# Performance work log

Measured on AMD Instinct MI355X. Metric: run time of the kernel, lower is better.

The kernel has to match this reference:

```python
import jax, jax.numpy as jnp
import numpy as np
from jax import lax

REPR_IN = (32, 16, 8)   # multiplicities of l=0,1,2 fields
SIZE = 5                # cubic kernel size (odd)
PAD = SIZE // 2


def setup_inputs() -> dict:
    key = jax.random.key(0)
    k1, k2 = jax.random.split(key)
    c_in = sum(mul * (2 * l + 1) for l, mul in enumerate(REPR_IN))   # 120
    n_non_scalar = sum(REPR_IN[1:])                                   # 24
    x = jax.random.normal(k1, (2, c_in, 48, 48, 48), dtype=jnp.float32)
    # SE3Convolution materialized as its effective dense conv kernel [O, I, D, H, W]
    fan_in = c_in * SIZE ** 3
    w_gate = jax.random.normal(k2, (n_non_scalar, c_in, SIZE, SIZE, SIZE), dtype=jnp.float32) / np.sqrt(fan_in)
    return {"x": x, "w_gate": w_gate}


def reference(x, w_gate):
    B, _, X, Y, Z = x.shape
    # Gate branch: 3D conv (same padding) -> sigmoid, one scalar gate per non-scalar field
    g = jax.nn.sigmoid(
        lax.conv_general_dilated(
            x, w_gate,
            window_strides=(1, 1, 1),
            padding=[(PAD, PAD)] * 3,
            dimension_numbers=("NCDHW", "OIDHW", "NCDHW"),
        )
    )  # [B, n_non_scalar, X, Y, Z]

    parts = []
    begin_x = 0
    begin_g = 0
    for l, mul in enumerate(REPR_IN):
        if mul == 0:
            continue
        dim = 2 * l + 1
        field_x = x[:, begin_x:begin_x + mul * dim]
        if l == 0:
            # scalar activation on the l=0 block
            parts.append(jax.nn.relu(field_x))
        else:
            # broadcast gate over the 2l+1 components of each field copy
            fx = field_x.reshape(B, mul, dim, X, Y, Z)
            fg = g[:, begin_g:begin_g + mul][:, :, None]      # [B, mul, 1, X, Y, Z]
            begin_g += mul
            parts.append((fx * fg).reshape(B, mul * dim, X, Y, Z))
        begin_x += mul * dim
    return jnp.concatenate(parts, axis=1)
```

## Files before the change

kernel.cpp:

```cpp
#include <hip/hip_runtime.h>

typedef __attribute__((ext_vector_type(8))) short short8;
typedef __attribute__((ext_vector_type(4))) float f32x4;

#define SDIM 48
#define SS   (48*48)
#define SSS  (48*48*48)
#define CIN  120
#define CIP  128
#define NCO  24
#define ZP   52
#define NTAP 125

#define WP_USHORTS (4*25*5*32*32)
#define WP_BYTES   ((size_t)WP_USHORTS*2)
#define XT_USHORTS ((size_t)2*48*48*ZP*CIP)
#define XT_BYTES   (XT_USHORTS*2)
#define WTOT_F32   (NCO*CIN*NTAP)

#define A_CHUNKS 1664
#define ABUF_USH 13312
#define GLP      25

__device__ __forceinline__ unsigned short f2bf(float f){
    unsigned u = __float_as_uint(f);
    u = (u + 0x7FFFu + ((u >> 16) & 1u)) >> 16;
    return (unsigned short)u;
}

__device__ __forceinline__ void gload_lds16(const unsigned short* g, unsigned short* l)
{
    __builtin_amdgcn_global_load_lds(
        (const __attribute__((address_space(1))) unsigned int*)g,
        (__attribute__((address_space(3))) unsigned int*)l,
        16, 0, 0);
}


__global__ __launch_bounds__(256)
void transpose_x(const float* __restrict__ x, unsigned short* __restrict__ xt)
{
    __shared__ unsigned short sm[CIN*50];
    int bid = blockIdx.x;
    const int iy = bid % 48; bid /= 48;
    const int ix = bid % 48;
    const int b  = bid / 48;
    const int tid = threadIdx.x;

    const float* __restrict__ src = x + (size_t)b*CIN*SSS + ((size_t)ix*48 + iy)*48;
    for (int idx = tid; idx < CIN*48; idx += 256) {
        int ci = idx / 48, z = idx - ci*48;
        sm[ci*50 + z] = f2bf(src[(size_t)ci*SSS + z]);
    }
    __syncthreads();
    unsigned short* __restrict__ dst = xt + (((size_t)(b*48 + ix)*48) + iy)*ZP*CIP;
    for (int odx = tid; odx < ZP*CIP; odx += 256) {
        int zp = odx >> 7, ci = odx & 127;
        int z = zp - 2;
        unsigned short v = 0;
        if (ci < CIN && (unsigned)z < 48u) v = sm[ci*50 + z];
        dst[odx] = v;
    }
}

__global__ __launch_bounds__(256)
void repack_w_bf16(const float* __restrict__ w, unsigned short* __restrict__ wp)
{
    int idx = blockIdx.x*256 + threadIdx.x;
    if (idx >= WP_USHORTS) return;
    int cik = idx & 31;
    int co  = (idx >> 5) & 31;
    int dz  = (idx >> 10) % 5;
    int t   = (idx / 5120) % 25;
    int cc  = idx / 128000;
    int ci  = cc*32 + cik;
    float v = 0.f;
    if (co < NCO && ci < CIN)
        v = w[(size_t)(co*CIN + ci)*NTAP + t*5 + dz];
    wp[idx] = f2bf(v);
}

#define MFMA16(a,b,c) __builtin_amdgcn_mfma_f32_16x16x32_bf16(a,b,c,0,0,0)

__global__ __launch_bounds__(128, 3)
void conv_mfma(const unsigned short* __restrict__ xt,
               const unsigned short* __restrict__ wp,
               const float* __restrict__ x,
               float* __restrict__ out)
{
    __shared__ __align__(16) unsigned short As[ABUF_USH];

    int bid = (blockIdx.x & 7) * 144 + (blockIdx.x >> 3);
    const int oyq = bid % 12; bid /= 12;
    const int ox = bid % 48;
    const int b  = bid / 48;

    const int tid = threadIdx.x;
    const int wave = tid >> 6, lane = tid & 63;
    const int l15 = lane & 15, l4 = lane >> 4;
    const int iy0 = oyq*4 - 2;

    const int dxlo = (ox < 2) ? (2 - ox) : 0;
    const int dxhi = (ox > 45) ? (49 - ox) : 4;
    const int ndx  = dxhi - dxlo + 1;

    int goff[13];
    bool ok[13];
#pragma unroll
    for (int k = 0; k < 13; ++k) {
        int L = k*128 + tid;
        int iyl = L / 208, r = L - iyl*208;
        int zp = r >> 2, sf = r & 3;
        int sg = sf ^ ((zp >> 1) & 3);
        int iy = iy0 + iyl;
        ok[k]   = (unsigned)iy < 48u;
        goff[k] = (iy*52 + zp)*128 + sg*8;
    }
    const unsigned short* zsrc = xt + (lane & 31)*8;

    f32x4 acc[2][3][2];
#pragma unroll
    for (int oh = 0; oh < 2; ++oh)
#pragma unroll
      for (int zb = 0; zb < 3; ++zb)
#pragma unroll
        for (int nt = 0; nt < 2; ++nt) acc[oh][zb][nt] = (f32x4){0,0,0,0};

#pragma unroll 1
    for (int cc = 0; cc < 4; ++cc) {
#pragma unroll 1
      for (int dxi = 0; dxi < ndx; ++dxi) {
        const int dx = dxlo + dxi;
        const int ix = ox + dx - 2;
        const unsigned short* __restrict__ slab =
            xt + (size_t)(b*48 + ix)*(48*52*128) + cc*32;

        __syncthreads();
#pragma unroll
        for (int k = 0; k < 13; ++k) {
            const unsigned short* src = ok[k] ? (slab + goff[k]) : zsrc;
            gload_lds16(src, As + k*1024 + wave*512);
        }
        asm volatile("s_waitcnt vmcnt(0)" ::: "memory");
        __builtin_amdgcn_sched_barrier(0);
        __syncthreads();

        const unsigned short* __restrict__ wdxb =
            wp + (size_t)cc*128000 + (size_t)dx*25600 + l15*32 + l4*8;
        const char* __restrict__ asb = (const char*)As;
#pragma unroll
        for (int dz = 0; dz < 5; ++dz) {
            short8 bb[5][2];
#pragma unroll
            for (int dy = 0; dy < 5; ++dy) {
                bb[dy][0] = *(const short8*)(wdxb + dy*5120 + dz*1024);
                bb[dy][1] = *(const short8*)(wdxb + dy*5120 + dz*1024 + 512);
            }
#pragma unroll
            for (int r = 0; r < 6; ++r) {
                const char* __restrict__ ab = asb + (wave*2 + r)*3328;
                short8 a[3];
#pragma unroll
                for (int zb = 0; zb < 3; ++zb) {
                    const int zp = l15 + dz + zb*16;
                    const int off = zp*64 + ((l4 ^ ((zp >> 1) & 3)) << 4);
                    a[zb] = *(const short8*)(ab + off);
                }
                if (r <= 4) {
#pragma unroll
                    for (int zb = 0; zb < 3; ++zb) {
                        acc[0][zb][0] = MFMA16(a[zb], bb[r][0], acc[0][zb][0]);
                        acc[0][zb][1] = MFMA16(a[zb], bb[r][1], acc[0][zb][1]);
                    }
                }
                if (r >= 1) {
#pragma unroll
                    for (int zb = 0; zb < 3; ++zb) {
                        acc[1][zb][0] = MFMA16(a[zb], bb[r-1][0], acc[1][zb][0]);
                        acc[1][zb][1] = MFMA16(a[zb], bb[r-1][1], acc[1][zb][1]);
                    }
                }
            }
        }
      }
    }

    __syncthreads();
    float* gl = (float*)As;

#pragma unroll
    for (int nt = 0; nt < 2; ++nt) {
        const int co = nt*16 + l15;
        if (co < NCO) {
#pragma unroll
            for (int oh = 0; oh < 2; ++oh)
#pragma unroll
              for (int zb = 0; zb < 3; ++zb)
#pragma unroll
                for (int r = 0; r < 4; ++r) {
                    const int z0 = zb*16 + l4*4 + r;
                    gl[((wave*2 + oh)*48 + z0)*GLP + co] =
                        1.f / (1.f + __expf(-acc[oh][zb][nt][r]));
                }
        }
    }
    __syncthreads();

    for (int i = tid; i < 384; i += 128) {
        const int pnt = i % 192;
        const int half = i / 192;
        const int z = pnt % 48, oyl = pnt / 48;
        const int oy2 = oyq*4 + oyl;
        const size_t sp = ((size_t)ox*48 + oy2)*48 + z;
        const float* __restrict__ xsp = x   + (size_t)b*CIN*SSS + sp;
        float*       __restrict__ osp = out + (size_t)b*CIN*SSS + sp;
        const float* __restrict__ gp = gl + pnt*GLP;
        for (int c = half*60; c < half*60 + 60; ++c) {
            float v = xsp[(size_t)c*SSS];
            float o;
            if (c < 32)       o = v > 0.f ? v : 0.f;
            else if (c < 80)  o = v * gp[(c - 32) / 3];
            else              o = v * gp[16 + (c - 80) / 5];
            osp[(size_t)c*SSS] = o;
        }
    }
}


__global__ __launch_bounds__(256)
void repack_w_f32(const float* __restrict__ w, float* __restrict__ wpf)
{
    int idx = blockIdx.x * 256 + threadIdx.x;
    if (idx >= WTOT_F32) return;
    int co = idx % NCO;
    int t  = idx / NCO;
    wpf[idx] = w[co * (CIN * NTAP) + t];
}

__global__ __launch_bounds__(128)
void gated_act_f32(const float* __restrict__ x,
                   const float* __restrict__ wpf,
                   float* __restrict__ out)
{
    const int gid = blockIdx.x * 128 + threadIdx.x;
    const int oz = gid % SDIM;
    int r = gid / SDIM;
    const int oy = r % SDIM; r /= SDIM;
    const int ox = r % SDIM;
    const int b  = r / SDIM;

    const float* __restrict__ xb = x + (size_t)b * CIN * SSS;
    float acc[NCO];
#pragma unroll
    for (int i = 0; i < NCO; ++i) acc[i] = 0.f;

    int izc[5]; bool okz[5];
#pragma unroll
    for (int dz = 0; dz < 5; ++dz) {
        int iz = oz + dz - 2;
        okz[dz] = (unsigned)iz < (unsigned)SDIM;
        izc[dz] = okz[dz] ? iz : 0;
    }
    for (int ci = 0; ci < CIN; ++ci) {
        const float* __restrict__ xc = xb + (size_t)ci * SSS;
        const float* __restrict__ wc = wpf + ci * (NTAP * NCO);
#pragma unroll 1
        for (int dx = 0; dx < 5; ++dx) {
            const int ix = ox + dx - 2;
            const bool okx = (unsigned)ix < (unsigned)SDIM;
            const int ixc = okx ? ix : 0;
#pragma unroll 1
            for (int dy = 0; dy < 5; ++dy) {
                const int iy = oy + dy - 2;
                const bool oky = (unsigned)iy < (unsigned)SDIM;
                const int iyc = oky ? iy : 0;
                const bool okxy = okx && oky;
                const float* __restrict__ xrow = xc + ixc * SS + iyc * SDIM;
                float xv[5];
#pragma unroll
                for (int dz = 0; dz < 5; ++dz) {
                    float v = xrow[izc[dz]];
                    xv[dz] = (okxy && okz[dz]) ? v : 0.f;
                }
                const float* __restrict__ wr = wc + (dx * 25 + dy * 5) * NCO;
#pragma unroll
                for (int dz = 0; dz < 5; ++dz) {
                    const float v = xv[dz];
#pragma unroll
                    for (int co = 0; co < NCO; ++co)
                        acc[co] = fmaf(v, wr[dz * NCO + co], acc[co]);
                }
            }
        }
    }
    float g[NCO];
#pragma unroll
    for (int co = 0; co < NCO; ++co)
        g[co] = 1.f / (1.f + __expf(-acc[co]));

    const size_t sbase = (size_t)b * CIN * SSS + ox * SS + oy * SDIM + oz;
    float* __restrict__ ob = out + sbase;
    const float* __restrict__ xs = x + sbase;
#pragma unroll
    for (int c = 0; c < 32; ++c) {
        float v = xs[(size_t)c * SSS];
        ob[(size_t)c * SSS] = v > 0.f ? v : 0.f;
    }
#pragma unroll
    for (int m = 0; m < 16; ++m) {
        const float gv = g[m];
#pragma unroll
        for (int k = 0; k < 3; ++k) {
            const int c = 32 + m * 3 + k;
            ob[(size_t)c * SSS] = xs[(size_t)c * SSS] * gv;
        }
    }
#pragma unroll
    for (int m = 0; m < 8; ++m) {
        const float gv = g[16 + m];
#pragma unroll
        for (int k = 0; k < 5; ++k) {
            const int c = 80 + m * 5 + k;
            ob[(size_t)c * SSS] = xs[(size_t)c * SSS] * gv;
        }
    }
}

extern "C" void kernel_launch(void* const* d_in, const int* in_sizes, int n_in,
                              void* d_out, int out_size, void* d_ws, size_t ws_size,
                              hipStream_t stream)
{
    const float* x = (const float*)d_in[0];
    const float* w = (const float*)d_in[1];
    float* out = (float*)d_out;

    if (ws_size >= WP_BYTES + XT_BYTES) {
        unsigned short* wp  = (unsigned short*)d_ws;
        unsigned short* xtb = (unsigned short*)((char*)d_ws + WP_BYTES);
        hipLaunchKernelGGL(repack_w_bf16, dim3((WP_USHORTS + 255) / 256), dim3(256),
                           0, stream, w, wp);
        hipLaunchKernelGGL(transpose_x, dim3(2*48*48), dim3(256), 0, stream, x, xtb);
        hipLaunchKernelGGL(conv_mfma, dim3(2*48*12), dim3(128), 0, stream,
                           xtb, wp, x, out);
    } else if (ws_size >= (size_t)WTOT_F32 * 4) {
        float* wpf = (float*)d_ws;
        hipLaunchKernelGGL(repack_w_f32, dim3((WTOT_F32 + 255) / 256), dim3(256),
                           0, stream, w, wpf);
        hipLaunchKernelGGL(gated_act_f32, dim3(2*SSS/128), dim3(128), 0, stream,
                           x, wpf, out);
    }
}
```

Baseline: 319.9 us.

## Use single-wave conv blocks and drop block barriers in the staging loop

Each conv block shrinks from two waves covering four output rows to one wave covering two rows, doubling the grid to 2304 blocks. With a single wave per block the __syncthreads around the LDS staging go away. The next slab is now issued right after the MFMA work, and s_setprio raises wave priority during the MFMA section. The cost is more redundant halo rows and weight loads per output row. There is still only one LDS buffer, so loads overlap compute only across different waves, not within a block.

After: 452.7 us. +41.5%, slower.

```diff
diff --git a/kernel.cpp b/kernel.cpp
--- a/kernel.cpp
+++ b/kernel.cpp
@@ -18,8 +18,8 @@
 #define XT_BYTES   (XT_USHORTS*2)
 #define WTOT_F32   (NCO*CIN*NTAP)
 
-#define A_CHUNKS 1664
-#define ABUF_USH 13312
+#define A_CHUNKS 1248
+#define AS_USH   10240
 #define GLP      25
 
 __device__ __forceinline__ unsigned short f2bf(float f){
@@ -82,72 +82,75 @@
 
 #define MFMA16(a,b,c) __builtin_amdgcn_mfma_f32_16x16x32_bf16(a,b,c,0,0,0)
 
-__global__ __launch_bounds__(128, 3)
+#define STAGE1(cc_, dx_) do {                                              \
+    const int ix_ = ox + (dx_) - 2;                                        \
+    const unsigned short* __restrict__ slab_ =                             \
+        xt + (size_t)(b*48 + ix_)*(48*52*128) + (cc_)*32;                  \
+    _Pragma("unroll")                                                      \
+    for (int k_ = 0; k_ < 20; ++k_) {                                      \
+        const unsigned short* src_ = ok[k_] ? (slab_ + goff[k_]) : zsrc;   \
+        gload_lds16(src_, As + k_*512);                                    \
+    }                                                                      \
+} while (0)
+
+__global__ __launch_bounds__(64, 2)
 void conv_mfma(const unsigned short* __restrict__ xt,
                const unsigned short* __restrict__ wp,
                const float* __restrict__ x,
                float* __restrict__ out)
 {
-    __shared__ __align__(16) unsigned short As[ABUF_USH];
-
-    int bid = (blockIdx.x & 7) * 144 + (blockIdx.x >> 3);
-    const int oyq = bid % 12; bid /= 12;
+    __shared__ __align__(16) unsigned short As[AS_USH];
+
+    int bid = (blockIdx.x & 7) * 288 + (blockIdx.x >> 3);
+    const int oyp = bid % 24; bid /= 24;
     const int ox = bid % 48;
     const int b  = bid / 48;
-
-    const int tid = threadIdx.x;
-    const int wave = tid >> 6, lane = tid & 63;
+    const int oy0 = oyp*2;
+
+    const int lane = threadIdx.x & 63;
     const int l15 = lane & 15, l4 = lane >> 4;
-    const int iy0 = oyq*4 - 2;
 
     const int dxlo = (ox < 2) ? (2 - ox) : 0;
     const int dxhi = (ox > 45) ? (49 - ox) : 4;
     const int ndx  = dxhi - dxlo + 1;
 
-    int goff[13];
-    bool ok[13];
-#pragma unroll
-    for (int k = 0; k < 13; ++k) {
-        int L = k*128 + tid;
-        int iyl = L / 208, r = L - iyl*208;
-        int zp = r >> 2, sf = r & 3;
+    int goff[20];
+    bool ok[20];
+#pragma unroll
+    for (int k = 0; k < 20; ++k) {
+        int L = k*64 + lane;
+        int row = L / 208, rem = L - row*208;
+        int zp = rem >> 2, sf = rem & 3;
         int sg = sf ^ ((zp >> 1) & 3);
-        int iy = iy0 + iyl;
-        ok[k]   = (unsigned)iy < 48u;
+        int iy = oy0 - 2 + row;
+        ok[k]   = (L < A_CHUNKS) && ((unsigned)iy < 48u);
         goff[k] = (iy*52 + zp)*128 + sg*8;
     }
     const unsigned short* zsrc = xt + (lane & 31)*8;
 
     f32x4 acc[2][3][2];
 #pragma unroll
-    for (int oh = 0; oh < 2; ++oh)
+    for (int ol = 0; ol < 2; ++ol)
 #pragma unroll
       for (int zb = 0; zb < 3; ++zb)
 #pragma unroll
-        for (int nt = 0; nt < 2; ++nt) acc[oh][zb][nt] = (f32x4){0,0,0,0};
+        for (int nt = 0; nt < 2; ++nt) acc[ol][zb][nt] = (f32x4){0,0,0,0};
+
+    STAGE1(0, dxlo);
 
 #pragma unroll 1
     for (int cc = 0; cc < 4; ++cc) {
 #pragma unroll 1
       for (int dxi = 0; dxi < ndx; ++dxi) {
         const int dx = dxlo + dxi;
-        const int ix = ox + dx - 2;
-        const unsigned short* __restrict__ slab =
-            xt + (size_t)(b*48 + ix)*(48*52*128) + cc*32;
-
-        __syncthreads();
-#pragma unroll
-        for (int k = 0; k < 13; ++k) {
-            const unsigned short* src = ok[k] ? (slab + goff[k]) : zsrc;
-            gload_lds16(src, As + k*1024 + wave*512);
-        }
+
         asm volatile("s_waitcnt vmcnt(0)" ::: "memory");
         __builtin_amdgcn_sched_barrier(0);
-        __syncthreads();
 
         const unsigned short* __restrict__ wdxb =
             wp + (size_t)cc*128000 + (size_t)dx*25600 + l15*32 + l4*8;
         const char* __restrict__ asb = (const char*)As;
+        __builtin_amdgcn_s_setprio(1);
 #pragma unroll
         for (int dz = 0; dz < 5; ++dz) {
             short8 bb[5][2];
@@ -158,7 +161,7 @@
             }
 #pragma unroll
             for (int r = 0; r < 6; ++r) {
-                const char* __restrict__ ab = asb + (wave*2 + r)*3328;
+                const char* __restrict__ ab = asb + r*3328;
                 short8 a[3];
 #pragma unroll
                 for (int zb = 0; zb < 3; ++zb) {
@@ -182,6 +185,16 @@
                 }
             }
         }
+        __builtin_amdgcn_s_setprio(0);
+
+        asm volatile("s_waitcnt lgkmcnt(0)" ::: "memory");
+        __builtin_amdgcn_sched_barrier(0);
+        {
+            const int more = (dxi + 1 < ndx);
+            const int cc2 = more ? cc : cc + 1;
+            const int dx2 = more ? dx + 1 : dxlo;
+            if (cc2 < 4) STAGE1(cc2, dx2);
+        }
       }
     }
 
@@ -193,24 +206,24 @@
         const int co = nt*16 + l15;
         if (co < NCO) {
 #pragma unroll
-            for (int oh = 0; oh < 2; ++oh)
+            for (int ol = 0; ol < 2; ++ol)
 #pragma unroll
               for (int zb = 0; zb < 3; ++zb)
 #pragma unroll
                 for (int r = 0; r < 4; ++r) {
                     const int z0 = zb*16 + l4*4 + r;
-                    gl[((wave*2 + oh)*48 + z0)*GLP + co] =
-                        1.f / (1.f + __expf(-acc[oh][zb][nt][r]));
+                    gl[(ol*48 + z0)*GLP + co] =
+                        1.f / (1.f + __expf(-acc[ol][zb][nt][r]));
                 }
         }
     }
     __syncthreads();
 
-    for (int i = tid; i < 384; i += 128) {
-        const int pnt = i % 192;
-        const int half = i / 192;
-        const int z = pnt % 48, oyl = pnt / 48;
-        const int oy2 = oyq*4 + oyl;
+    for (int i = lane; i < 192; i += 64) {
+        const int pnt = i % 96;
+        const int half = i / 96;
+        const int z = pnt % 48, ol = pnt / 48;
+        const int oy2 = oy0 + ol;
         const size_t sp = ((size_t)ox*48 + oy2)*48 + z;
         const float* __restrict__ xsp = x   + (size_t)b*CIN*SSS + sp;
         float*       __restrict__ osp = out + (size_t)b*CIN*SSS + sp;
@@ -340,7 +353,7 @@
         hipLaunchKernelGGL(repack_w_bf16, dim3((WP_USHORTS + 255) / 256), dim3(256),
                            0, stream, w, wp);
         hipLaunchKernelGGL(transpose_x, dim3(2*48*48), dim3(256), 0, stream, x, xtb);
-        hipLaunchKernelGGL(conv_mfma, dim3(2*48*12), dim3(128), 0, stream,
+        hipLaunchKernelGGL(conv_mfma, dim3(2*48*24), dim3(64), 0, stream,
                            xtb, wp, x, out);
     } else if (ws_size >= (size_t)WTOT_F32 * 4) {
         float* wpf = (float*)d_ws;
```

## Enlarge conv output tile to six y-rows per block, three per wave

Applied to the files above, without the earlier changes.

Each block now computes 6 output y-rows instead of 4, with each wave accumulating 3 rows. The LDS input slab grows from 8 to 10 y-rows, so each loaded slab and each set of weight fragments feeds more MFMAs. This cuts the halo overhead per output and the number of blocks from 1152 to 768. In exchange it uses more accumulator registers and LDS, which may lower occupancy under launch_bounds(128,3), and it leaves fewer blocks to spread across the CUs.

After: 334.6 us. +4.6%, slower.

```diff
diff --git a/kernel.cpp b/kernel.cpp
--- a/kernel.cpp
+++ b/kernel.cpp
@@ -18,8 +18,8 @@
 #define XT_BYTES   (XT_USHORTS*2)
 #define WTOT_F32   (NCO*CIN*NTAP)
 
-#define A_CHUNKS 1664
-#define ABUF_USH 13312
+#define A_CHUNKS 2080
+#define AS_USH   16896
 #define GLP      25
 
 __device__ __forceinline__ unsigned short f2bf(float f){
@@ -88,43 +88,43 @@
                const float* __restrict__ x,
                float* __restrict__ out)
 {
-    __shared__ __align__(16) unsigned short As[ABUF_USH];
-
-    int bid = (blockIdx.x & 7) * 144 + (blockIdx.x >> 3);
-    const int oyq = bid % 12; bid /= 12;
+    __shared__ __align__(16) unsigned short As[AS_USH];
+
+    int bid = (blockIdx.x & 7) * 96 + (blockIdx.x >> 3);
+    const int oyg = bid % 8; bid /= 8;
     const int ox = bid % 48;
     const int b  = bid / 48;
 
     const int tid = threadIdx.x;
     const int wave = tid >> 6, lane = tid & 63;
     const int l15 = lane & 15, l4 = lane >> 4;
-    const int iy0 = oyq*4 - 2;
+    const int iy0 = oyg*6 - 2;
 
     const int dxlo = (ox < 2) ? (2 - ox) : 0;
     const int dxhi = (ox > 45) ? (49 - ox) : 4;
     const int ndx  = dxhi - dxlo + 1;
 
-    int goff[13];
-    bool ok[13];
-#pragma unroll
-    for (int k = 0; k < 13; ++k) {
+    int goff[17];
+    bool ok[17];
+#pragma unroll
+    for (int k = 0; k < 17; ++k) {
         int L = k*128 + tid;
-        int iyl = L / 208, r = L - iyl*208;
-        int zp = r >> 2, sf = r & 3;
+        int row = L / 208, rem = L - row*208;
+        int zp = rem >> 2, sf = rem & 3;
         int sg = sf ^ ((zp >> 1) & 3);
-        int iy = iy0 + iyl;
-        ok[k]   = (unsigned)iy < 48u;
+        int iy = iy0 + row;
+        ok[k]   = (L < A_CHUNKS) && ((unsigned)iy < 48u);
         goff[k] = (iy*52 + zp)*128 + sg*8;
     }
     const unsigned short* zsrc = xt + (lane & 31)*8;
 
-    f32x4 acc[2][3][2];
-#pragma unroll
-    for (int oh = 0; oh < 2; ++oh)
+    f32x4 acc[3][3][2];
+#pragma unroll
+    for (int ol = 0; ol < 3; ++ol)
 #pragma unroll
       for (int zb = 0; zb < 3; ++zb)
 #pragma unroll
-        for (int nt = 0; nt < 2; ++nt) acc[oh][zb][nt] = (f32x4){0,0,0,0};
+        for (int nt = 0; nt < 2; ++nt) acc[ol][zb][nt] = (f32x4){0,0,0,0};
 
 #pragma unroll 1
     for (int cc = 0; cc < 4; ++cc) {
@@ -137,9 +137,13 @@
 
         __syncthreads();
 #pragma unroll
-        for (int k = 0; k < 13; ++k) {
+        for (int k = 0; k < 16; ++k) {
             const unsigned short* src = ok[k] ? (slab + goff[k]) : zsrc;
             gload_lds16(src, As + k*1024 + wave*512);
+        }
+        if (wave == 0) {
+            const unsigned short* src = ok[16] ? (slab + goff[16]) : zsrc;
+            gload_lds16(src, As + 16*1024);
         }
         asm volatile("s_waitcnt vmcnt(0)" ::: "memory");
         __builtin_amdgcn_sched_barrier(0);
@@ -157,8 +161,8 @@
                 bb[dy][1] = *(const short8*)(wdxb + dy*5120 + dz*1024 + 512);
             }
 #pragma unroll
-            for (int r = 0; r < 6; ++r) {
-                const char* __restrict__ ab = asb + (wave*2 + r)*3328;
+            for (int r = 0; r < 7; ++r) {
+                const char* __restrict__ ab = asb + (wave*3 + r)*3328;
                 short8 a[3];
 #pragma unroll
                 for (int zb = 0; zb < 3; ++zb) {
@@ -166,18 +170,15 @@
                     const int off = zp*64 + ((l4 ^ ((zp >> 1) & 3)) << 4);
                     a[zb] = *(const short8*)(ab + off);
                 }
-                if (r <= 4) {
-#pragma unroll
-                    for (int zb = 0; zb < 3; ++zb) {
-                        acc[0][zb][0] = MFMA16(a[zb], bb[r][0], acc[0][zb][0]);
-                        acc[0][zb][1] = MFMA16(a[zb], bb[r][1], acc[0][zb][1]);
-                    }
-                }
-                if (r >= 1) {
-#pragma unroll
-                    for (int zb = 0; zb < 3; ++zb) {
-                        acc[1][zb][0] = MFMA16(a[zb], bb[r-1][0], acc[1][zb][0]);
-                        acc[1][zb][1] = MFMA16(a[zb], bb[r-1][1], acc[1][zb][1]);
+#pragma unroll
+                for (int ol = 0; ol < 3; ++ol) {
+                    const int dy = r - ol;
+                    if (dy >= 0 && dy <= 4) {
+#pragma unroll
+                        for (int zb = 0; zb < 3; ++zb) {
+                            acc[ol][zb][0] = MFMA16(a[zb], bb[dy][0], acc[ol][zb][0]);
+                            acc[ol][zb][1] = MFMA16(a[zb], bb[dy][1], acc[ol][zb][1]);
+                        }
                     }
                 }
             }
@@ -193,24 +194,24 @@
         const int co = nt*16 + l15;
         if (co < NCO) {
 #pragma unroll
-            for (int oh = 0; oh < 2; ++oh)
+            for (int ol = 0; ol < 3; ++ol)
 #pragma unroll
               for (int zb = 0; zb < 3; ++zb)
 #pragma unroll
                 for (int r = 0; r < 4; ++r) {
                     const int z0 = zb*16 + l4*4 + r;
-                    gl[((wave*2 + oh)*48 + z0)*GLP + co] =
-                        1.f / (1.f + __expf(-acc[oh][zb][nt][r]));
+                    gl[((wave*3 + ol)*48 + z0)*GLP + co] =
+                        1.f / (1.f + __expf(-acc[ol][zb][nt][r]));
                 }
         }
     }
     __syncthreads();
 
-    for (int i = tid; i < 384; i += 128) {
-        const int pnt = i % 192;
-        const int half = i / 192;
+    for (int i = tid; i < 576; i += 128) {
+        const int pnt = i % 288;
+        const int half = i / 288;
         const int z = pnt % 48, oyl = pnt / 48;
-        const int oy2 = oyq*4 + oyl;
+        const int oy2 = oyg*6 + oyl;
         const size_t sp = ((size_t)ox*48 + oy2)*48 + z;
         const float* __restrict__ xsp = x   + (size_t)b*CIN*SSS + sp;
         float*       __restrict__ osp = out + (size_t)b*CIN*SSS + sp;
@@ -340,7 +341,7 @@
         hipLaunchKernelGGL(repack_w_bf16, dim3((WP_USHORTS + 255) / 256), dim3(256),
                            0, stream, w, wp);
         hipLaunchKernelGGL(transpose_x, dim3(2*48*48), dim3(256), 0, stream, x, xtb);
-        hipLaunchKernelGGL(conv_mfma, dim3(2*48*12), dim3(128), 0, stream,
+        hipLaunchKernelGGL(conv_mfma, dim3(2*48*8), dim3(128), 0, stream,
                            xtb, wp, x, out);
     } else if (ws_size >= (size_t)WTOT_F32 * 4) {
         float* wpf = (float*)d_ws;
```

## Split input-channel reduction across two wave pairs per block with LDS reduce

Applied to the files above, without the earlier changes.

Doubles the block to 256 threads and gives each pair of waves half of the input-channel chunks, each with its own LDS staging buffer. The partial conv sums are written to LDS, then added together before the sigmoid in the epilogue. This shortens the serial channel loop per wave and raises wave-level parallelism per output tile, at the cost of twice the LDS per block, fewer co-resident blocks, and an extra reduction step. It also raises wave priority with s_setprio around the MFMA section.

After: 323.9 us. No clear change (+1.3%).

```diff
diff --git a/kernel.cpp b/kernel.cpp
--- a/kernel.cpp
+++ b/kernel.cpp
@@ -82,13 +82,13 @@
 
 #define MFMA16(a,b,c) __builtin_amdgcn_mfma_f32_16x16x32_bf16(a,b,c,0,0,0)
 
-__global__ __launch_bounds__(128, 3)
+__global__ __launch_bounds__(256, 3)
 void conv_mfma(const unsigned short* __restrict__ xt,
                const unsigned short* __restrict__ wp,
                const float* __restrict__ x,
                float* __restrict__ out)
 {
-    __shared__ __align__(16) unsigned short As[ABUF_USH];
+    __shared__ __align__(16) unsigned short As[2*ABUF_USH];
 
     int bid = (blockIdx.x & 7) * 144 + (blockIdx.x >> 3);
     const int oyq = bid % 12; bid /= 12;
@@ -96,7 +96,10 @@
     const int b  = bid / 48;
 
     const int tid = threadIdx.x;
-    const int wave = tid >> 6, lane = tid & 63;
+    const int pair = tid >> 7;
+    const int ptid = tid & 127;
+    const int wol  = (tid >> 6) & 1;
+    const int lane = tid & 63;
     const int l15 = lane & 15, l4 = lane >> 4;
     const int iy0 = oyq*4 - 2;
 
@@ -108,16 +111,18 @@
     bool ok[13];
 #pragma unroll
     for (int k = 0; k < 13; ++k) {
-        int L = k*128 + tid;
-        int iyl = L / 208, r = L - iyl*208;
-        int zp = r >> 2, sf = r & 3;
+        int L = k*128 + ptid;
+        int row = L / 208, rem = L - row*208;
+        int zp = rem >> 2, sf = rem & 3;
         int sg = sf ^ ((zp >> 1) & 3);
-        int iy = iy0 + iyl;
+        int iy = iy0 + row;
         ok[k]   = (unsigned)iy < 48u;
         goff[k] = (iy*52 + zp)*128 + sg*8;
     }
     const unsigned short* zsrc = xt + (lane & 31)*8;
 
+    unsigned short* __restrict__ Asp = As + pair*ABUF_USH;
+
     f32x4 acc[2][3][2];
 #pragma unroll
     for (int oh = 0; oh < 2; ++oh)
@@ -127,7 +132,8 @@
         for (int nt = 0; nt < 2; ++nt) acc[oh][zb][nt] = (f32x4){0,0,0,0};
 
 #pragma unroll 1
-    for (int cc = 0; cc < 4; ++cc) {
+    for (int icc = 0; icc < 2; ++icc) {
+      const int cc = pair*2 + icc;
 #pragma unroll 1
       for (int dxi = 0; dxi < ndx; ++dxi) {
         const int dx = dxlo + dxi;
@@ -139,7 +145,7 @@
 #pragma unroll
         for (int k = 0; k < 13; ++k) {
             const unsigned short* src = ok[k] ? (slab + goff[k]) : zsrc;
-            gload_lds16(src, As + k*1024 + wave*512);
+            gload_lds16(src, Asp + k*1024 + wol*512);
         }
         asm volatile("s_waitcnt vmcnt(0)" ::: "memory");
         __builtin_amdgcn_sched_barrier(0);
@@ -147,7 +153,8 @@
 
         const unsigned short* __restrict__ wdxb =
             wp + (size_t)cc*128000 + (size_t)dx*25600 + l15*32 + l4*8;
-        const char* __restrict__ asb = (const char*)As;
+        const char* __restrict__ asb = (const char*)Asp;
+        __builtin_amdgcn_s_setprio(1);
 #pragma unroll
         for (int dz = 0; dz < 5; ++dz) {
             short8 bb[5][2];
@@ -158,7 +165,7 @@
             }
 #pragma unroll
             for (int r = 0; r < 6; ++r) {
-                const char* __restrict__ ab = asb + (wave*2 + r)*3328;
+                const char* __restrict__ ab = asb + (wol*2 + r)*3328;
                 short8 a[3];
 #pragma unroll
                 for (int zb = 0; zb < 3; ++zb) {
@@ -182,12 +189,14 @@
                 }
             }
         }
+        __builtin_amdgcn_s_setprio(0);
       }
     }
 
     __syncthreads();
     float* gl = (float*)As;
 
+    float* __restrict__ glp = gl + pair*(192*GLP);
 #pragma unroll
     for (int nt = 0; nt < 2; ++nt) {
         const int co = nt*16 + l15;
@@ -199,14 +208,13 @@
 #pragma unroll
                 for (int r = 0; r < 4; ++r) {
                     const int z0 = zb*16 + l4*4 + r;
-                    gl[((wave*2 + oh)*48 + z0)*GLP + co] =
-                        1.f / (1.f + __expf(-acc[oh][zb][nt][r]));
+                    glp[((wol*2 + oh)*48 + z0)*GLP + co] = acc[oh][zb][nt][r];
                 }
         }
     }
     __syncthreads();
 
-    for (int i = tid; i < 384; i += 128) {
+    for (int i = tid; i < 384; i += 256) {
         const int pnt = i % 192;
         const int half = i / 192;
         const int z = pnt % 48, oyl = pnt / 48;
@@ -214,13 +222,18 @@
         const size_t sp = ((size_t)ox*48 + oy2)*48 + z;
         const float* __restrict__ xsp = x   + (size_t)b*CIN*SSS + sp;
         float*       __restrict__ osp = out + (size_t)b*CIN*SSS + sp;
-        const float* __restrict__ gp = gl + pnt*GLP;
+        const float* __restrict__ gp0 = gl + pnt*GLP;
+        const float* __restrict__ gp1 = gl + 192*GLP + pnt*GLP;
         for (int c = half*60; c < half*60 + 60; ++c) {
             float v = xsp[(size_t)c*SSS];
             float o;
-            if (c < 32)       o = v > 0.f ? v : 0.f;
-            else if (c < 80)  o = v * gp[(c - 32) / 3];
-            else              o = v * gp[16 + (c - 80) / 5];
+            if (c < 32) {
+                o = v > 0.f ? v : 0.f;
+            } else {
+                const int gi = (c < 80) ? (c - 32) / 3 : 16 + (c - 80) / 5;
+                const float gv = 1.f / (1.f + __expf(-(gp0[gi] + gp1[gi])));
+                o = v * gv;
+            }
             osp[(size_t)c*SSS] = o;
         }
     }
@@ -340,7 +353,7 @@
         hipLaunchKernelGGL(repack_w_bf16, dim3((WP_USHORTS + 255) / 256), dim3(256),
                            0, stream, w, wp);
         hipLaunchKernelGGL(transpose_x, dim3(2*48*48), dim3(256), 0, stream, x, xtb);
-        hipLaunchKernelGGL(conv_mfma, dim3(2*48*12), dim3(128), 0, stream,
+        hipLaunchKernelGGL(conv_mfma, dim3(2*48*12), dim3(256), 0, stream,
                            xtb, wp, x, out);
     } else if (ws_size >= (size_t)WTOT_F32 * 4) {
         float* wpf = (float*)d_ws;
```
